# Kernel optimization log

Hardware: AMD Instinct MI355X
Metric: run time of the kernel (lower is better)

The kernel has to match this reference:

```python
import jax, jax.numpy as jnp
import numpy as np

R = 2            # radix
N = 1024         # input_size (power of R)
DEPTH = 10       # log_R(N) levels
SIZES = [N >> l for l in range(DEPTH)]                 # per-level input_size: 1024,512,...,2
OFFSETS = np.concatenate([[0], np.cumsum(SIZES)])      # offsets into flat butterfly-weight vector
TOTAL_W = int(OFFSETS[-1])                             # 2046
# residual cascade in the torch code: int(True)-1 = 0 (False), int(0)-1 = -1 -> bool(-1)=True,
# and it stays truthy for all deeper levels.
RES = [True, False] + [True] * (DEPTH - 2)


def setup_inputs() -> dict:
    key = jax.random.key(0)
    k1, k2, k3 = jax.random.split(key, 3)
    x = jax.random.normal(k1, (4, 4096, N), dtype=jnp.float32)
    bw = jax.random.normal(k2, (TOTAL_W,), dtype=jnp.float32) * 0.1   # xavier-ish scale
    lw = jax.random.normal(k3, (DEPTH, R, R), dtype=jnp.float32) * 0.5
    return {"x": x, "bw": bw, "lw": lw}


def _fft(x, bw, lw, level):
    """One DIT radix-R butterfly level applied to the last dim of x (eval mode: dropout = id)."""
    n = x.shape[-1]                                   # input_size at this level
    o = int(OFFSETS[level])
    w = bw[o:o + n].reshape(R, n // R)                # elementwise 'twiddle' weights (r, n/r)
    xr = x.reshape(x.shape[:-1] + (R, n // R))        # (..., r, n/r)
    inner = _fft(xr, bw, lw, level + 1) if n > R else xr   # recurse on last dim n/r; Identity at base
    # torch: einsum('ij,...ik->...jk', lin_weights, weights * recursive(x))
    y = jnp.einsum('ij,...ik->...jk', lw[level], w * inner).reshape(x.shape)
    return x + y if RES[level] else y


def reference(x, bw, lw):
    return _fft(x, bw, lw, 0)
```

## Files before the change

kernel.cpp:

```cpp
#include <hip/hip_runtime.h>


constexpr int VECLEN = 1024;

__device__ __forceinline__ int swz(int f) {
  return f ^ (((f >> 5) & 7) << 2);
}

template<int L, bool RESL>
__device__ __forceinline__ void level_inlane(float (&v)[16], const float (&xr)[16],
                                             const float* __restrict__ bw,
                                             const float* __restrict__ lw) {
  constexpr int n = VECLEN >> L;
  constexpr int h = n >> 1;
  constexpr int off = 2048 - (2048 >> L);
  float w[n];
#pragma unroll
  for (int i = 0; i < n; ++i) w[i] = bw[off + i];
  const float l00 = lw[L*4+0], l01 = lw[L*4+1], l10 = lw[L*4+2], l11 = lw[L*4+3];
#pragma unroll
  for (int r = 0; r < 16; ++r) {
    if ((r & h) == 0) {
      const int q = r ^ h;
      const float t0 = w[r & (n-1)] * v[r];
      const float t1 = w[q & (n-1)] * v[q];
      const float y0 = l00*t0 + l10*t1;
      const float y1 = l01*t0 + l11*t1;
      v[r] = RESL ? xr[r] + y0 : y0;
      v[q] = RESL ? xr[q] + y1 : y1;
    }
  }
}

template<int L, bool RESL>
__device__ __forceinline__ void level_dpp(float (&v)[16], const float (&xr)[16],
                                          const float (&w)[16],
                                          const float* __restrict__ lw, int lane) {
  static_assert(L == 4 || L == 5, "DPP levels only");
  constexpr int ctl = (L == 5) ? 0xB1 : 0x4E;
  const int role = (lane >> (5 - L)) & 1;
  const float l00 = lw[L*4+0], l01 = lw[L*4+1], l10 = lw[L*4+2], l11 = lw[L*4+3];
  const float cs = role ? l11 : l00;
  const float cp = role ? l01 : l10;
#pragma unroll
  for (int r = 0; r < 16; ++r) {
    const float t = w[r] * v[r];
    const float tp = __int_as_float(
        __builtin_amdgcn_update_dpp(0, __float_as_int(t), ctl, 0xF, 0xF, true));
    const float y = cs*t + cp*tp;
    v[r] = RESL ? xr[r] + y : y;
  }
}

template<int L>
__device__ __forceinline__ void loadw_A(float (&w)[16], const float* lds_bw, int lane) {
  constexpr int n = VECLEN >> L;
  constexpr int off = 2048 - (2048 >> L);
  const int f0 = off + ((lane * 16) & (n - 1));
#pragma unroll
  for (int k = 0; k < 4; ++k) {
    const float4 f = *reinterpret_cast<const float4*>(lds_bw + swz(f0 + 4*k));
    w[4*k+0]=f.x; w[4*k+1]=f.y; w[4*k+2]=f.z; w[4*k+3]=f.w;
  }
}

template<int L>
__device__ __forceinline__ void loadw_B(float* w, const float* lds_bw, int lane) {
  constexpr int off = 2048 - (2048 >> L);
  constexpr int nr = (VECLEN >> L) >> 6;
#pragma unroll
  for (int j = 0; j < nr; ++j)
    w[j] = lds_bw[swz(off + j*64 + lane)];
}

template<int L, bool RESL>
__device__ __forceinline__ void level_B(float (&v)[16], const float (&xr)[16],
                                        const float* w, const float* __restrict__ lw) {
  constexpr int nr = (VECLEN >> L) >> 6;
  constexpr int hb = nr >> 1;
  const float l00 = lw[L*4+0], l01 = lw[L*4+1], l10 = lw[L*4+2], l11 = lw[L*4+3];
#pragma unroll
  for (int r = 0; r < 16; ++r) {
    if ((r & hb) == 0) {
      const int q = r ^ hb;
      const float t0 = w[r & (nr-1)] * v[r];
      const float t1 = w[q & (nr-1)] * v[q];
      const float y0 = l00*t0 + l10*t1;
      const float y1 = l01*t0 + l11*t1;
      v[r] = RESL ? xr[r] + y0 : y0;
      v[q] = RESL ? xr[q] + y1 : y1;
    }
  }
}

__global__ __launch_bounds__(256)
void rnnfft_kernel(const float* __restrict__ x,
                   const float* __restrict__ bw,
                   const float* __restrict__ lw,
                   float* __restrict__ out, int nvec) {
  __shared__ float lds_bw[2048];
  __shared__ float tbuf[4][1024];
  const int t = threadIdx.x;
  const int w4 = t >> 6;
  const int lane = t & 63;
  const int wid = blockIdx.x * 4 + w4;
  const size_t base = (size_t)wid * VECLEN;
  float* buf = tbuf[w4];

  float v[16], xr[16];
#pragma unroll
  for (int k = 0; k < 4; ++k) {
    const float4 f = *reinterpret_cast<const float4*>(x + base + lane*16 + 4*k);
    xr[4*k+0]=f.x; xr[4*k+1]=f.y; xr[4*k+2]=f.z; xr[4*k+3]=f.w;
  }

#pragma unroll
  for (int k = 0; k < 4; ++k) {
    float4 f;
    f.x = xr[4*k+0]; f.y = xr[4*k+1]; f.z = xr[4*k+2]; f.w = xr[4*k+3];
    *reinterpret_cast<float4*>(buf + swz(lane*16 + 4*k)) = f;
  }

  if (t < 252) {
    const float4 a = *reinterpret_cast<const float4*>(bw + 8*t);
    const float4 b = *reinterpret_cast<const float4*>(bw + 8*t + 4);
    *reinterpret_cast<float4*>(lds_bw + swz(8*t)) = a;
    *reinterpret_cast<float4*>(lds_bw + swz(8*t+4)) = b;
  }
  __syncthreads();

#pragma unroll
  for (int r = 0; r < 16; ++r) v[r] = xr[r];

  float wA[16], wB[16];
  loadw_A<5>(wA, lds_bw, lane);
  loadw_A<4>(wB, lds_bw, lane);

  level_inlane<9, true>(v, xr, bw, lw);
  level_inlane<8, true>(v, xr, bw, lw);
  level_inlane<7, true>(v, xr, bw, lw);
  level_inlane<6, true>(v, xr, bw, lw);
  level_dpp<5, true>(v, xr, wA, lw, lane);
  level_dpp<4, true>(v, xr, wB, lw, lane);

  float xrB[16];
#pragma unroll
  for (int r = 0; r < 16; ++r) xrB[r] = buf[swz(r*64 + lane)];

#pragma unroll
  for (int k = 0; k < 4; ++k) {
    float4 f;
    f.x = v[4*k+0]; f.y = v[4*k+1]; f.z = v[4*k+2]; f.w = v[4*k+3];
    *reinterpret_cast<float4*>(buf + swz(lane*16 + 4*k)) = f;
  }

  float w3[2], w2[4], w1[8], w0[16];
  loadw_B<3>(w3, lds_bw, lane);
  loadw_B<2>(w2, lds_bw, lane);

#pragma unroll
  for (int r = 0; r < 16; ++r) v[r] = buf[swz(r*64 + lane)];

  level_B<3, true >(v, xrB, w3, lw);
  loadw_B<1>(w1, lds_bw, lane);
  level_B<2, true >(v, xrB, w2, lw);
  loadw_B<0>(w0, lds_bw, lane);
  level_B<1, false>(v, xrB, w1, lw);
  level_B<0, true >(v, xrB, w0, lw);

#pragma unroll
  for (int r = 0; r < 16; ++r)
    __builtin_nontemporal_store(v[r], &out[base + r*64 + lane]);
}

extern "C" void kernel_launch(void* const* d_in, const int* in_sizes, int n_in,
                              void* d_out, int out_size, void* d_ws, size_t ws_size,
                              hipStream_t stream) {
  const float* x  = (const float*)d_in[0];
  const float* bw = (const float*)d_in[1];
  const float* lw = (const float*)d_in[2];
  float* out = (float*)d_out;
  const int nvec = in_sizes[0] / VECLEN;
  const int wpb = 4;
  const int blocks = (nvec + wpb - 1) / wpb;
  rnnfft_kernel<<<blocks, 256, 0, stream>>>(x, bw, lw, out, nvec);
}
```

Measured before the change: 29.48 us.

## Process two vectors per wave and prefetch second input during first

Each wave now handles two 1024-element vectors instead of one, halving the grid size. The second vector's global load is issued before phase B of the first vector runs, so load latency can overlap with compute. The per-block bw staging into LDS is also amortized over twice the work. The cost is more live registers and fewer waves in flight, which can reduce the latency hiding that occupancy provided. The code assumes an even vector count and has no bounds check.

Measured after the change: 30.39 us. +3.1%, slower.

```diff
diff --git a/kernel.cpp b/kernel.cpp
--- a/kernel.cpp
+++ b/kernel.cpp
@@ -91,6 +91,49 @@
       v[q] = RESL ? xr[q] + y1 : y1;
     }
   }
+}
+
+__device__ __forceinline__ void loadX_A(float (&xr)[16], const float* __restrict__ x,
+                                        size_t base, int lane) {
+#pragma unroll
+  for (int k = 0; k < 4; ++k) {
+    const float4 f = *reinterpret_cast<const float4*>(x + base + lane*16 + 4*k);
+    xr[4*k+0]=f.x; xr[4*k+1]=f.y; xr[4*k+2]=f.z; xr[4*k+3]=f.w;
+  }
+}
+
+__device__ __forceinline__ void phaseA_and_writeV(float (&v)[16], const float (&xr)[16],
+                                                  float* buf, const float* lds_bw,
+                                                  const float* __restrict__ bw,
+                                                  const float* __restrict__ lw, int lane) {
+  float wA[16], wB[16];
+  loadw_A<5>(wA, lds_bw, lane);
+  loadw_A<4>(wB, lds_bw, lane);
+  level_inlane<9, true>(v, xr, bw, lw);
+  level_inlane<8, true>(v, xr, bw, lw);
+  level_inlane<7, true>(v, xr, bw, lw);
+  level_inlane<6, true>(v, xr, bw, lw);
+  level_dpp<5, true>(v, xr, wA, lw, lane);
+  level_dpp<4, true>(v, xr, wB, lw, lane);
+}
+
+__device__ __forceinline__ void phaseB_and_store(float (&v)[16], const float (&xrB)[16],
+                                                 const float* lds_bw,
+                                                 const float* __restrict__ lw,
+                                                 float* __restrict__ out,
+                                                 size_t base, int lane) {
+  float w3[2], w2[4], w1[8], w0[16];
+  loadw_B<3>(w3, lds_bw, lane);
+  loadw_B<2>(w2, lds_bw, lane);
+  level_B<3, true >(v, xrB, w3, lw);
+  loadw_B<1>(w1, lds_bw, lane);
+  level_B<2, true >(v, xrB, w2, lw);
+  loadw_B<0>(w0, lds_bw, lane);
+  level_B<1, false>(v, xrB, w1, lw);
+  level_B<0, true >(v, xrB, w0, lw);
+#pragma unroll
+  for (int r = 0; r < 16; ++r)
+    __builtin_nontemporal_store(v[r], &out[base + r*64 + lane]);
 }
 
 __global__ __launch_bounds__(256)
@@ -104,16 +147,12 @@
   const int w4 = t >> 6;
   const int lane = t & 63;
   const int wid = blockIdx.x * 4 + w4;
-  const size_t base = (size_t)wid * VECLEN;
+  const size_t baseA = (size_t)(2 * wid) * VECLEN;
+  const size_t baseB = baseA + VECLEN;
   float* buf = tbuf[w4];
 
   float v[16], xr[16];
-#pragma unroll
-  for (int k = 0; k < 4; ++k) {
-    const float4 f = *reinterpret_cast<const float4*>(x + base + lane*16 + 4*k);
-    xr[4*k+0]=f.x; xr[4*k+1]=f.y; xr[4*k+2]=f.z; xr[4*k+3]=f.w;
-  }
-
+  loadX_A(xr, x, baseA, lane);
 #pragma unroll
   for (int k = 0; k < 4; ++k) {
     float4 f;
@@ -131,22 +170,11 @@
 
 #pragma unroll
   for (int r = 0; r < 16; ++r) v[r] = xr[r];
-
-  float wA[16], wB[16];
-  loadw_A<5>(wA, lds_bw, lane);
-  loadw_A<4>(wB, lds_bw, lane);
-
-  level_inlane<9, true>(v, xr, bw, lw);
-  level_inlane<8, true>(v, xr, bw, lw);
-  level_inlane<7, true>(v, xr, bw, lw);
-  level_inlane<6, true>(v, xr, bw, lw);
-  level_dpp<5, true>(v, xr, wA, lw, lane);
-  level_dpp<4, true>(v, xr, wB, lw, lane);
+  phaseA_and_writeV(v, xr, buf, lds_bw, bw, lw, lane);
 
   float xrB[16];
 #pragma unroll
   for (int r = 0; r < 16; ++r) xrB[r] = buf[swz(r*64 + lane)];
-
 #pragma unroll
   for (int k = 0; k < 4; ++k) {
     float4 f;
@@ -154,23 +182,34 @@
     *reinterpret_cast<float4*>(buf + swz(lane*16 + 4*k)) = f;
   }
 
-  float w3[2], w2[4], w1[8], w0[16];
-  loadw_B<3>(w3, lds_bw, lane);
-  loadw_B<2>(w2, lds_bw, lane);
+  float xn[16];
+  loadX_A(xn, x, baseB, lane);
 
 #pragma unroll
   for (int r = 0; r < 16; ++r) v[r] = buf[swz(r*64 + lane)];
-
-  level_B<3, true >(v, xrB, w3, lw);
-  loadw_B<1>(w1, lds_bw, lane);
-  level_B<2, true >(v, xrB, w2, lw);
-  loadw_B<0>(w0, lds_bw, lane);
-  level_B<1, false>(v, xrB, w1, lw);
-  level_B<0, true >(v, xrB, w0, lw);
-
-#pragma unroll
-  for (int r = 0; r < 16; ++r)
-    __builtin_nontemporal_store(v[r], &out[base + r*64 + lane]);
+  phaseB_and_store(v, xrB, lds_bw, lw, out, baseA, lane);
+
+#pragma unroll
+  for (int k = 0; k < 4; ++k) {
+    float4 f;
+    f.x = xn[4*k+0]; f.y = xn[4*k+1]; f.z = xn[4*k+2]; f.w = xn[4*k+3];
+    *reinterpret_cast<float4*>(buf + swz(lane*16 + 4*k)) = f;
+  }
+#pragma unroll
+  for (int r = 0; r < 16; ++r) v[r] = xn[r];
+  phaseA_and_writeV(v, xn, buf, lds_bw, bw, lw, lane);
+
+#pragma unroll
+  for (int r = 0; r < 16; ++r) xrB[r] = buf[swz(r*64 + lane)];
+#pragma unroll
+  for (int k = 0; k < 4; ++k) {
+    float4 f;
+    f.x = v[4*k+0]; f.y = v[4*k+1]; f.z = v[4*k+2]; f.w = v[4*k+3];
+    *reinterpret_cast<float4*>(buf + swz(lane*16 + 4*k)) = f;
+  }
+#pragma unroll
+  for (int r = 0; r < 16; ++r) v[r] = buf[swz(r*64 + lane)];
+  phaseB_and_store(v, xrB, lds_bw, lw, out, baseB, lane);
 }
 
 extern "C" void kernel_launch(void* const* d_in, const int* in_sizes, int n_in,
@@ -181,7 +220,8 @@
   const float* lw = (const float*)d_in[2];
   float* out = (float*)d_out;
   const int nvec = in_sizes[0] / VECLEN;
+  const int nwave = nvec / 2;
   const int wpb = 4;
-  const int blocks = (nvec + wpb - 1) / wpb;
+  const int blocks = (nwave + wpb - 1) / wpb;
   rnnfft_kernel<<<blocks, 256, 0, stream>>>(x, bw, lw, out, nvec);
 }
```
